# Kernel tuning notes

Hardware: AMD Instinct MI355X
Metric: run time of the kernel (lower is better)

## Reference

```python
import jax, jax.numpy as jnp
import numpy as np

B, T, D, A = 4, 4096, 1024, 64
RINGS = 2

def _build_graph_matrix(A, rings):
    # W[a_dst, a_src] = 1/len(neigh) for src in {a_dst-rings..a_dst+rings} within bounds (mean reduce)
    W = np.zeros((A, A), dtype=np.float32)
    for a in range(A):
        neigh = [n for n in range(a - rings, a + rings + 1) if 0 <= n < A]
        W[a, neigh] = 1.0 / len(neigh)
    return jnp.asarray(W)

def setup_inputs() -> dict:
    key = jax.random.key(0)
    k0, k1, k2 = jax.random.split(key, 3)
    x = jax.random.normal(k0, (B, T, D), dtype=jnp.float32)
    # contiguous-ish 1D region assignment of tokens to anchors
    assign = jnp.sort(jax.random.randint(k1, (T,), 0, A)).astype(jnp.int32)
    counts = jnp.clip(jnp.zeros((A,), jnp.float32).at[assign].add(1.0), 1.0, None)
    W_proj = jax.random.normal(k2, (D, D), dtype=jnp.float32) * (1.0 / np.sqrt(D))
    gate = jnp.float32(0.1)
    W_graph = _build_graph_matrix(A, RINGS)
    return {"x": x, "W_proj": W_proj, "gate": gate, "assign": assign,
            "W_graph": W_graph, "counts": counts, "hops": 1}

def reference(x, W_proj, gate, assign, W_graph, counts, hops):
    Bx, Tx, Dx = x.shape
    Ax = counts.shape[0]
    # pool_per_anchor (mean): scatter-add tokens into anchors, divide by counts
    anchor = jnp.zeros((Bx, Ax, Dx), x.dtype).at[:, assign, :].add(x)
    anchor = anchor / counts[None, :, None]
    # neighbor_aggregate: out = einsum('bcd,ac->bad', out, W) per hop
    agg = anchor
    for _ in range(max(1, int(hops))):
        agg = jnp.einsum('ac,bcd->bad', W_graph, agg)
    # broadcast_from_anchor: gather each token's anchor feature
    fb = agg[:, assign, :]  # [B,T,D]
    # residual with gated linear projection (dropout identity in eval)
    return x + (fb @ W_proj.T) * jnp.tanh(gate)
```

## Files before the change

kernel.cpp:

```cpp
#include <hip/hip_runtime.h>
#include <cmath>


typedef __attribute__((ext_vector_type(8))) short bf16x8;
typedef __attribute__((ext_vector_type(4))) float f32x4;

#define OROWS 8

__device__ inline short f2bf(float f) {
    unsigned u = __float_as_uint(f);
    return (short)((u + 0x7FFFu + ((u >> 16) & 1u)) >> 16);
}
__device__ inline int lbound(const int* __restrict__ a, int n, int v) {
    int lo = 0, hi = n;
    while (lo < hi) { int m = (lo + hi) >> 1; if (a[m] < v) lo = m + 1; else hi = m; }
    return lo;
}

__global__ __launch_bounds__(256) void prepanchor_kernel(
        const float* __restrict__ x, const float* __restrict__ counts,
        const int* __restrict__ assign, const float* __restrict__ Wg,
        const int* __restrict__ hops, const float* __restrict__ Wp,
        short* __restrict__ anchorb, short* __restrict__ Wpb, float* __restrict__ M,
        int T, int D, int A, int R) {
    __shared__ float s0[4096];
    __shared__ float s1[4096];
    int bid = blockIdx.x, tid = threadIdx.x;
    int rs = D >> 2;
    if (bid < R) {
        int b = bid / A, a = bid - (bid / A) * A;
        int* sT = (int*)s1;
        if (tid < 2) sT[tid] = lbound(assign, T, a + tid);
        __syncthreads();
        int t0 = sT[0], t1 = sT[1];
        float inv = 1.0f / counts[a];
        const float4* x4 = (const float4*)x + (size_t)b * T * rs;
        short4* an4 = (short4*)anchorb + (size_t)bid * rs;
        for (int d4 = tid; d4 < rs; d4 += 256) {
            float4 acc = make_float4(0.f, 0.f, 0.f, 0.f);
            const float4* p = x4 + (size_t)t0 * rs + d4;
            int t = t0;
            for (; t + 8 <= t1; t += 8) {
                float4 v0 = p[0];
                float4 v1 = p[(size_t)rs];
                float4 v2 = p[(size_t)2 * rs];
                float4 v3 = p[(size_t)3 * rs];
                float4 v4 = p[(size_t)4 * rs];
                float4 v5 = p[(size_t)5 * rs];
                float4 v6 = p[(size_t)6 * rs];
                float4 v7 = p[(size_t)7 * rs];
                acc.x += ((v0.x + v1.x) + (v2.x + v3.x)) + ((v4.x + v5.x) + (v6.x + v7.x));
                acc.y += ((v0.y + v1.y) + (v2.y + v3.y)) + ((v4.y + v5.y) + (v6.y + v7.y));
                acc.z += ((v0.z + v1.z) + (v2.z + v3.z)) + ((v4.z + v5.z) + (v6.z + v7.z));
                acc.w += ((v0.w + v1.w) + (v2.w + v3.w)) + ((v4.w + v5.w) + (v6.w + v7.w));
                p += (size_t)8 * rs;
            }
            for (; t < t1; ++t) {
                float4 v = *p;
                acc.x += v.x; acc.y += v.y; acc.z += v.z; acc.w += v.w;
                p += rs;
            }
            short4 o;
            o.x = f2bf(acc.x * inv); o.y = f2bf(acc.y * inv);
            o.z = f2bf(acc.z * inv); o.w = f2bf(acc.w * inv);
            an4[d4] = o;
        }
    } else if (bid < R + 256) {
        long long n8 = (long long)D * D / 8;
        for (long long i = (long long)(bid - R) * 256 + tid; i < n8; i += 256LL * 256LL) {
            const float4* p = (const float4*)Wp + i * 2;
            float4 v0 = p[0], v1 = p[1];
            short4* q = (short4*)Wpb + i * 2;
            short4 o0, o1;
            o0.x = f2bf(v0.x); o0.y = f2bf(v0.y); o0.z = f2bf(v0.z); o0.w = f2bf(v0.w);
            o1.x = f2bf(v1.x); o1.y = f2bf(v1.y); o1.z = f2bf(v1.z); o1.w = f2bf(v1.w);
            q[0] = o0; q[1] = o1;
        }
    } else {
        int n = A * A;
        for (int i = tid; i < n; i += 256) s0[i] = Wg[i];
        int h = hops[0]; if (h < 1) h = 1;
        for (int it = 1; it < h; ++it) {
            __syncthreads();
            for (int i = tid; i < n; i += 256) {
                int r = i / A, c = i - (i / A) * A;
                float s = 0.f;
                for (int k = 0; k < A; ++k) s += Wg[r * A + k] * s0[k * A + c];
                s1[i] = s;
            }
            __syncthreads();
            for (int i = tid; i < n; i += 256) s0[i] = s1[i];
        }
        __syncthreads();
        for (int i = tid; i < n; i += 256) M[i] = s0[i];
    }
}

__global__ __launch_bounds__(256) void zgemm_kernel(
        const short* __restrict__ Agb, const short* __restrict__ Wpb,
        float* __restrict__ Z, int D) {
    int wave = threadIdx.x >> 6;
    int lane = threadIdx.x & 63;
    int rBase = blockIdx.x * 16;
    int dBase = blockIdx.y * 64 + wave * 16;
    int rc = lane & 15;
    int kOff = (lane >> 4) * 8;
    const short* aPtr = Agb + (size_t)(rBase + rc) * D + kOff;
    const short* bPtr = Wpb + (size_t)(dBase + rc) * D + kOff;
    f32x4 acc = {0.f, 0.f, 0.f, 0.f};
    #pragma unroll 8
    for (int k = 0; k < D; k += 32) {
        bf16x8 af = *(const bf16x8*)(aPtr + k);
        bf16x8 bf = *(const bf16x8*)(bPtr + k);
        acc = __builtin_amdgcn_mfma_f32_16x16x32_bf16(af, bf, acc, 0, 0, 0);
    }
    int orow = (lane >> 4) * 4;
    #pragma unroll
    for (int j = 0; j < 4; ++j)
        Z[(size_t)(rBase + orow + j) * D + dBase + rc] = acc[j];
}

__global__ __launch_bounds__(256) void mix_kernel(
        const float* __restrict__ Z, const float* __restrict__ M,
        float* __restrict__ Y, int D, int A) {
    int b = blockIdx.x / A, a = blockIdx.x - (blockIdx.x / A) * A;
    __shared__ float row[64];
    if (threadIdx.x < A) row[threadIdx.x] = M[a * A + threadIdx.x];
    __syncthreads();
    int rs = D >> 2;
    const float4* z4 = (const float4*)Z + (size_t)b * A * rs;
    float4* y4 = (float4*)Y + (size_t)blockIdx.x * rs;
    for (int d4 = threadIdx.x; d4 < rs; d4 += 256) {
        float4 acc = make_float4(0.f, 0.f, 0.f, 0.f);
        for (int c = 0; c < A; ++c) {
            float w = row[c];
            float4 v = z4[(size_t)c * rs + d4];
            acc.x += w * v.x; acc.y += w * v.y; acc.z += w * v.z; acc.w += w * v.w;
        }
        y4[d4] = acc;
    }
}

__global__ __launch_bounds__(256) void out_kernel(
        const float* __restrict__ x, const float* __restrict__ Y,
        const int* __restrict__ assign, const float* __restrict__ gate,
        float* __restrict__ out, int T, int D, int A) {
    float tg = tanhf(gate[0]);
    int rs = D >> 2;
    int bt0 = blockIdx.x * OROWS;
    const float4* x4 = (const float4*)x;
    const float4* y4 = (const float4*)Y;
    float4* o4 = (float4*)out;
    #pragma unroll
    for (int r = 0; r < OROWS; ++r) {
        int bt = bt0 + r;
        int b = bt / T;
        int t = bt - b * T;
        int a = assign[t];
        const float4* yr = y4 + ((size_t)b * A + a) * rs;
        for (int d4 = threadIdx.x; d4 < rs; d4 += 256) {
            float4 xv = x4[(size_t)bt * rs + d4];
            float4 yv = yr[d4];
            o4[(size_t)bt * rs + d4] = make_float4(xv.x + tg * yv.x, xv.y + tg * yv.y,
                                                   xv.z + tg * yv.z, xv.w + tg * yv.w);
        }
    }
}

extern "C" void kernel_launch(void* const* d_in, const int* in_sizes, int n_in,
                              void* d_out, int out_size, void* d_ws, size_t ws_size,
                              hipStream_t stream) {
    const float* x      = (const float*)d_in[0];
    const float* Wp     = (const float*)d_in[1];
    const float* gate   = (const float*)d_in[2];
    const int*   assign = (const int*)d_in[3];
    const float* Wg     = (const float*)d_in[4];
    const float* counts = (const float*)d_in[5];
    const int*   hops   = (const int*)d_in[6];
    float* out = (float*)d_out;

    int T = in_sizes[3];
    int A = in_sizes[5];
    int D = (int)(sqrt((double)in_sizes[1]) + 0.5);
    int B = (int)(in_sizes[0] / ((long long)T * D));
    int R = B * A;

    float* Z       = (float*)d_ws;
    float* Y       = Z + (size_t)R * D;
    float* M       = Y + (size_t)R * D;
    short* anchorb = (short*)(M + (size_t)A * A);
    short* Wpb     = anchorb + (size_t)R * D;

    prepanchor_kernel<<<R + 257, 256, 0, stream>>>(x, counts, assign, Wg, hops, Wp,
                                                   anchorb, Wpb, M, T, D, A, R);
    dim3 g(R / 16, D / 64);
    zgemm_kernel<<<g, 256, 0, stream>>>(anchorb, Wpb, Z, D);
    mix_kernel<<<R, 256, 0, stream>>>(Z, M, Y, D, A);
    out_kernel<<<B * T / OROWS, 256, 0, stream>>>(x, Y, assign, gate, out, T, D, A);
}
```

Before: 60.09 us.

## Fuse projection GEMM, graph mix, and residual output into one kernel

```diff
diff --git a/kernel.cpp b/kernel.cpp
--- a/kernel.cpp
+++ b/kernel.cpp
@@ -5,7 +5,7 @@
 typedef __attribute__((ext_vector_type(8))) short bf16x8;
 typedef __attribute__((ext_vector_type(4))) float f32x4;
 
-#define OROWS 8
+#define CH 512
 
 __device__ inline short f2bf(float f) {
     unsigned u = __float_as_uint(f);
@@ -96,73 +96,96 @@
     }
 }
 
-__global__ __launch_bounds__(256) void zgemm_kernel(
-        const short* __restrict__ Agb, const short* __restrict__ Wpb,
-        float* __restrict__ Z, int D) {
-    int wave = threadIdx.x >> 6;
-    int lane = threadIdx.x & 63;
-    int rBase = blockIdx.x * 16;
-    int dBase = blockIdx.y * 64 + wave * 16;
-    int rc = lane & 15;
-    int kOff = (lane >> 4) * 8;
-    const short* aPtr = Agb + (size_t)(rBase + rc) * D + kOff;
-    const short* bPtr = Wpb + (size_t)(dBase + rc) * D + kOff;
-    f32x4 acc = {0.f, 0.f, 0.f, 0.f};
-    #pragma unroll 8
-    for (int k = 0; k < D; k += 32) {
-        bf16x8 af = *(const bf16x8*)(aPtr + k);
-        bf16x8 bf = *(const bf16x8*)(bPtr + k);
-        acc = __builtin_amdgcn_mfma_f32_16x16x32_bf16(af, bf, acc, 0, 0, 0);
-    }
-    int orow = (lane >> 4) * 4;
-    #pragma unroll
-    for (int j = 0; j < 4; ++j)
-        Z[(size_t)(rBase + orow + j) * D + dBase + rc] = acc[j];
-}
-
-__global__ __launch_bounds__(256) void mix_kernel(
-        const float* __restrict__ Z, const float* __restrict__ M,
-        float* __restrict__ Y, int D, int A) {
-    int b = blockIdx.x / A, a = blockIdx.x - (blockIdx.x / A) * A;
-    __shared__ float row[64];
-    if (threadIdx.x < A) row[threadIdx.x] = M[a * A + threadIdx.x];
+__global__ __launch_bounds__(256) void fused_kernel(
+        const float* __restrict__ x, const short* __restrict__ anchorb,
+        const short* __restrict__ Wpb, const float* __restrict__ M,
+        const int* __restrict__ assign, const float* __restrict__ gate,
+        float* __restrict__ out, int B, int T, int D, int A) {
+    __shared__ float Z_lds[64][68];
+    __shared__ float Y_lds[64][68];
+    __shared__ int a_lds[CH];
+    int b = blockIdx.x, dblk = blockIdx.y, tch = blockIdx.z;
+    int t0 = tch * CH;
+    int t1 = t0 + CH; if (t1 > T) t1 = T;
+    int len = t1 - t0;
+    int tid = threadIdx.x;
+    int wave = tid >> 6, lane = tid & 63;
+    int rc = lane & 15, kq = lane >> 4;
+    int cpair = wave >> 1, dpair = wave & 1;
+
+    for (int i = tid; i < len; i += 256) a_lds[i] = assign[t0 + i];
     __syncthreads();
-    int rs = D >> 2;
-    const float4* z4 = (const float4*)Z + (size_t)b * A * rs;
-    float4* y4 = (float4*)Y + (size_t)blockIdx.x * rs;
-    for (int d4 = threadIdx.x; d4 < rs; d4 += 256) {
-        float4 acc = make_float4(0.f, 0.f, 0.f, 0.f);
-        for (int c = 0; c < A; ++c) {
-            float w = row[c];
-            float4 v = z4[(size_t)c * rs + d4];
-            acc.x += w * v.x; acc.y += w * v.y; acc.z += w * v.z; acc.w += w * v.w;
-        }
-        y4[d4] = acc;
-    }
-}
-
-__global__ __launch_bounds__(256) void out_kernel(
-        const float* __restrict__ x, const float* __restrict__ Y,
-        const int* __restrict__ assign, const float* __restrict__ gate,
-        float* __restrict__ out, int T, int D, int A) {
+    int a_lo = a_lds[0], a_hi = a_lds[len - 1];
+    int nA = a_hi - a_lo + 1;
+
+    {
+        const short* aB0 = anchorb + (size_t)(b * A + cpair * 32 + rc) * D + kq * 8;
+        const short* aB1 = aB0 + (size_t)16 * D;
+        const short* bB0 = Wpb + (size_t)(dblk * 64 + dpair * 32 + rc) * D + kq * 8;
+        const short* bB1 = bB0 + (size_t)16 * D;
+        f32x4 acc00 = {0.f,0.f,0.f,0.f}, acc01 = {0.f,0.f,0.f,0.f};
+        f32x4 acc10 = {0.f,0.f,0.f,0.f}, acc11 = {0.f,0.f,0.f,0.f};
+        for (int k = 0; k < D; k += 32) {
+            bf16x8 a0 = *(const bf16x8*)(aB0 + k);
+            bf16x8 a1 = *(const bf16x8*)(aB1 + k);
+            bf16x8 b0 = *(const bf16x8*)(bB0 + k);
+            bf16x8 b1 = *(const bf16x8*)(bB1 + k);
+            acc00 = __builtin_amdgcn_mfma_f32_16x16x32_bf16(a0, b0, acc00, 0, 0, 0);
+            acc01 = __builtin_amdgcn_mfma_f32_16x16x32_bf16(a0, b1, acc01, 0, 0, 0);
+            acc10 = __builtin_amdgcn_mfma_f32_16x16x32_bf16(a1, b0, acc10, 0, 0, 0);
+            acc11 = __builtin_amdgcn_mfma_f32_16x16x32_bf16(a1, b1, acc11, 0, 0, 0);
+        }
+        int zr = cpair * 32 + kq * 4;
+        int zc = dpair * 32 + rc;
+        #pragma unroll
+        for (int j = 0; j < 4; ++j) {
+            Z_lds[zr + j][zc]           = acc00[j];
+            Z_lds[zr + j][zc + 16]      = acc01[j];
+            Z_lds[zr + 16 + j][zc]      = acc10[j];
+            Z_lds[zr + 16 + j][zc + 16] = acc11[j];
+        }
+    }
+    __syncthreads();
+
+    for (int i = tid; i < nA * 16; i += 256) {
+        int a_ = i >> 4, d4 = i & 15;
+        const float* Mrow = M + (size_t)(a_lo + a_) * A;
+        f32x4 acc = {0.f, 0.f, 0.f, 0.f};
+        for (int c = 0; c < 64; ++c) {
+            float w = Mrow[c];
+            f32x4 z = *(const f32x4*)&Z_lds[c][d4 * 4];
+            acc[0] += w * z[0]; acc[1] += w * z[1];
+            acc[2] += w * z[2]; acc[3] += w * z[3];
+        }
+        *(f32x4*)&Y_lds[a_][d4 * 4] = acc;
+    }
+    __syncthreads();
+
     float tg = tanhf(gate[0]);
-    int rs = D >> 2;
-    int bt0 = blockIdx.x * OROWS;
+    int rs4 = D >> 2;
     const float4* x4 = (const float4*)x;
-    const float4* y4 = (const float4*)Y;
     float4* o4 = (float4*)out;
-    #pragma unroll
-    for (int r = 0; r < OROWS; ++r) {
-        int bt = bt0 + r;
-        int b = bt / T;
-        int t = bt - b * T;
-        int a = assign[t];
-        const float4* yr = y4 + ((size_t)b * A + a) * rs;
-        for (int d4 = threadIdx.x; d4 < rs; d4 += 256) {
-            float4 xv = x4[(size_t)bt * rs + d4];
-            float4 yv = yr[d4];
-            o4[(size_t)bt * rs + d4] = make_float4(xv.x + tg * yv.x, xv.y + tg * yv.y,
-                                                   xv.z + tg * yv.z, xv.w + tg * yv.w);
+    size_t base = (size_t)(b * T + t0) * rs4 + dblk * 16;
+    if (len == CH) {
+        #pragma unroll 4
+        for (int i = tid; i < CH * 16; i += 256) {
+            int row = i >> 4, d4 = i & 15;
+            int a = a_lds[row] - a_lo;
+            size_t idx = base + (size_t)row * rs4 + d4;
+            float4 xv = x4[idx];
+            f32x4 yv = *(const f32x4*)&Y_lds[a][d4 * 4];
+            o4[idx] = make_float4(xv.x + tg * yv[0], xv.y + tg * yv[1],
+                                  xv.z + tg * yv[2], xv.w + tg * yv[3]);
+        }
+    } else {
+        for (int i = tid; i < len * 16; i += 256) {
+            int row = i >> 4, d4 = i & 15;
+            int a = a_lds[row] - a_lo;
+            size_t idx = base + (size_t)row * rs4 + d4;
+            float4 xv = x4[idx];
+            f32x4 yv = *(const f32x4*)&Y_lds[a][d4 * 4];
+            o4[idx] = make_float4(xv.x + tg * yv[0], xv.y + tg * yv[1],
+                                  xv.z + tg * yv[2], xv.w + tg * yv[3]);
         }
     }
 }
@@ -185,16 +208,13 @@
     int B = (int)(in_sizes[0] / ((long long)T * D));
     int R = B * A;
 
-    float* Z       = (float*)d_ws;
-    float* Y       = Z + (size_t)R * D;
-    float* M       = Y + (size_t)R * D;
+    float* M       = (float*)d_ws;
     short* anchorb = (short*)(M + (size_t)A * A);
     short* Wpb     = anchorb + (size_t)R * D;
 
     prepanchor_kernel<<<R + 257, 256, 0, stream>>>(x, counts, assign, Wg, hops, Wp,
                                                    anchorb, Wpb, M, T, D, A, R);
-    dim3 g(R / 16, D / 64);
-    zgemm_kernel<<<g, 256, 0, stream>>>(anchorb, Wpb, Z, D);
-    mix_kernel<<<R, 256, 0, stream>>>(Z, M, Y, D, A);
-    out_kernel<<<B * T / OROWS, 256, 0, stream>>>(x, Y, assign, gate, out, T, D, A);
-}
+    dim3 g(B, D / 64, (T + CH - 1) / CH);
+    fused_kernel<<<g, 256, 0, stream>>>(x, anchorb, Wpb, M, assign, gate, out,
+                                        B, T, D, A);
+}
```

Result: slower. 72.06 us (+19.9%).

## Fuse projection GEMM with graph mixing and fold gate and counts into mix matrix

Applied to the files above, without the earlier changes.

```diff
diff --git a/kernel.cpp b/kernel.cpp
--- a/kernel.cpp
+++ b/kernel.cpp
@@ -17,11 +17,12 @@
     return lo;
 }
 
-__global__ __launch_bounds__(256) void prepanchor_kernel(
+__global__ __launch_bounds__(256) void prep_kernel(
         const float* __restrict__ x, const float* __restrict__ counts,
         const int* __restrict__ assign, const float* __restrict__ Wg,
         const int* __restrict__ hops, const float* __restrict__ Wp,
-        short* __restrict__ anchorb, short* __restrict__ Wpb, float* __restrict__ M,
+        const float* __restrict__ gate,
+        short* __restrict__ anchorb, short* __restrict__ Wpb, float* __restrict__ Mp,
         int T, int D, int A, int R) {
     __shared__ float s0[4096];
     __shared__ float s1[4096];
@@ -33,7 +34,6 @@
         if (tid < 2) sT[tid] = lbound(assign, T, a + tid);
         __syncthreads();
         int t0 = sT[0], t1 = sT[1];
-        float inv = 1.0f / counts[a];
         const float4* x4 = (const float4*)x + (size_t)b * T * rs;
         short4* an4 = (short4*)anchorb + (size_t)bid * rs;
         for (int d4 = tid; d4 < rs; d4 += 256) {
@@ -61,8 +61,8 @@
                 p += rs;
             }
             short4 o;
-            o.x = f2bf(acc.x * inv); o.y = f2bf(acc.y * inv);
-            o.z = f2bf(acc.z * inv); o.w = f2bf(acc.w * inv);
+            o.x = f2bf(acc.x); o.y = f2bf(acc.y);
+            o.z = f2bf(acc.z); o.w = f2bf(acc.w);
             an4[d4] = o;
         }
     } else if (bid < R + 256) {
@@ -92,60 +92,56 @@
             for (int i = tid; i < n; i += 256) s0[i] = s1[i];
         }
         __syncthreads();
-        for (int i = tid; i < n; i += 256) M[i] = s0[i];
+        float tg = tanhf(gate[0]);
+        for (int i = tid; i < n; i += 256) {
+            int c = i - (i / A) * A;
+            Mp[i] = tg * s0[i] / counts[c];
+        }
     }
 }
 
-__global__ __launch_bounds__(256) void zgemm_kernel(
-        const short* __restrict__ Agb, const short* __restrict__ Wpb,
-        float* __restrict__ Z, int D) {
-    int wave = threadIdx.x >> 6;
-    int lane = threadIdx.x & 63;
-    int rBase = blockIdx.x * 16;
-    int dBase = blockIdx.y * 64 + wave * 16;
-    int rc = lane & 15;
-    int kOff = (lane >> 4) * 8;
-    const short* aPtr = Agb + (size_t)(rBase + rc) * D + kOff;
-    const short* bPtr = Wpb + (size_t)(dBase + rc) * D + kOff;
+__global__ __launch_bounds__(256) void zmix_kernel(
+        const short* __restrict__ anchorb, const short* __restrict__ Wpb,
+        const float* __restrict__ Mp, float* __restrict__ Y, int D, int A) {
+    __shared__ float Z_lds[64][20];
+    int b = blockIdx.x, dblk = blockIdx.y;
+    int tid = threadIdx.x;
+    int wave = tid >> 6, lane = tid & 63;
+    int rc = lane & 15, kq = lane >> 4;
+
+    const short* aP = anchorb + (size_t)(b * A + wave * 16 + rc) * D + kq * 8;
+    const short* bP = Wpb + (size_t)(dblk * 16 + rc) * D + kq * 8;
     f32x4 acc = {0.f, 0.f, 0.f, 0.f};
     #pragma unroll 8
     for (int k = 0; k < D; k += 32) {
-        bf16x8 af = *(const bf16x8*)(aPtr + k);
-        bf16x8 bf = *(const bf16x8*)(bPtr + k);
-        acc = __builtin_amdgcn_mfma_f32_16x16x32_bf16(af, bf, acc, 0, 0, 0);
+        bf16x8 av = *(const bf16x8*)(aP + k);
+        bf16x8 bv = *(const bf16x8*)(bP + k);
+        acc = __builtin_amdgcn_mfma_f32_16x16x32_bf16(av, bv, acc, 0, 0, 0);
     }
-    int orow = (lane >> 4) * 4;
+    int zr = wave * 16 + kq * 4;
     #pragma unroll
     for (int j = 0; j < 4; ++j)
-        Z[(size_t)(rBase + orow + j) * D + dBase + rc] = acc[j];
-}
+        Z_lds[zr + j][rc] = acc[j];
+    __syncthreads();
 
-__global__ __launch_bounds__(256) void mix_kernel(
-        const float* __restrict__ Z, const float* __restrict__ M,
-        float* __restrict__ Y, int D, int A) {
-    int b = blockIdx.x / A, a = blockIdx.x - (blockIdx.x / A) * A;
-    __shared__ float row[64];
-    if (threadIdx.x < A) row[threadIdx.x] = M[a * A + threadIdx.x];
-    __syncthreads();
-    int rs = D >> 2;
-    const float4* z4 = (const float4*)Z + (size_t)b * A * rs;
-    float4* y4 = (float4*)Y + (size_t)blockIdx.x * rs;
-    for (int d4 = threadIdx.x; d4 < rs; d4 += 256) {
-        float4 acc = make_float4(0.f, 0.f, 0.f, 0.f);
-        for (int c = 0; c < A; ++c) {
-            float w = row[c];
-            float4 v = z4[(size_t)c * rs + d4];
-            acc.x += w * v.x; acc.y += w * v.y; acc.z += w * v.z; acc.w += w * v.w;
-        }
-        y4[d4] = acc;
+    int a_ = tid >> 2, dq = tid & 3;
+    const float* Mrow = Mp + (size_t)a_ * A;
+    f32x4 ym = {0.f, 0.f, 0.f, 0.f};
+    #pragma unroll 8
+    for (int c = 0; c < 64; ++c) {
+        float w = Mrow[c];
+        ym[0] += w * Z_lds[c][dq * 4 + 0];
+        ym[1] += w * Z_lds[c][dq * 4 + 1];
+        ym[2] += w * Z_lds[c][dq * 4 + 2];
+        ym[3] += w * Z_lds[c][dq * 4 + 3];
     }
+    *(f32x4*)&Y[((size_t)b * A + a_) * D + dblk * 16 + dq * 4] = ym;
 }
 
 __global__ __launch_bounds__(256) void out_kernel(
         const float* __restrict__ x, const float* __restrict__ Y,
-        const int* __restrict__ assign, const float* __restrict__ gate,
-        float* __restrict__ out, int T, int D, int A) {
-    float tg = tanhf(gate[0]);
+        const int* __restrict__ assign, float* __restrict__ out,
+        int T, int D, int A) {
     int rs = D >> 2;
     int bt0 = blockIdx.x * OROWS;
     const float4* x4 = (const float4*)x;
@@ -161,8 +157,8 @@
         for (int d4 = threadIdx.x; d4 < rs; d4 += 256) {
             float4 xv = x4[(size_t)bt * rs + d4];
             float4 yv = yr[d4];
-            o4[(size_t)bt * rs + d4] = make_float4(xv.x + tg * yv.x, xv.y + tg * yv.y,
-                                                   xv.z + tg * yv.z, xv.w + tg * yv.w);
+            o4[(size_t)bt * rs + d4] = make_float4(xv.x + yv.x, xv.y + yv.y,
+                                                   xv.z + yv.z, xv.w + yv.w);
         }
     }
 }
@@ -185,16 +181,14 @@
     int B = (int)(in_sizes[0] / ((long long)T * D));
     int R = B * A;
 
-    float* Z       = (float*)d_ws;
-    float* Y       = Z + (size_t)R * D;
-    float* M       = Y + (size_t)R * D;
-    short* anchorb = (short*)(M + (size_t)A * A);
+    float* Mp      = (float*)d_ws;
+    float* Y       = Mp + (size_t)A * A;
+    short* anchorb = (short*)(Y + (size_t)R * D);
     short* Wpb     = anchorb + (size_t)R * D;
 
-    prepanchor_kernel<<<R + 257, 256, 0, stream>>>(x, counts, assign, Wg, hops, Wp,
-                                                   anchorb, Wpb, M, T, D, A, R);
-    dim3 g(R / 16, D / 64);
-    zgemm_kernel<<<g, 256, 0, stream>>>(anchorb, Wpb, Z, D);
-    mix_kernel<<<R, 256, 0, stream>>>(Z, M, Y, D, A);
-    out_kernel<<<B * T / OROWS, 256, 0, stream>>>(x, Y, assign, gate, out, T, D, A);
+    prep_kernel<<<R + 257, 256, 0, stream>>>(x, counts, assign, Wg, hops, Wp, gate,
+                                             anchorb, Wpb, Mp, T, D, A, R);
+    dim3 g(B, D / 16);
+    zmix_kernel<<<g, 256, 0, stream>>>(anchorb, Wpb, Mp, Y, D, A);
+    out_kernel<<<B * T / OROWS, 256, 0, stream>>>(x, Y, assign, out, T, D, A);
 }
```

Result: faster. 53.31 us (-11.3%).
